# Kernel optimization log

Hardware: AMD Instinct MI355X
Metric: run time of the kernel (lower is better)

The kernel has to match this reference:

```python
import jax, jax.numpy as jnp
import numpy as np

ALPHA = 0.2  # LeakyReLU negative slope
NEG_INF = -9e15


def setup_inputs() -> dict:
    key = jax.random.key(0)
    k1, k2, k3, k4, k5 = jax.random.split(key, 5)
    B, N, F_in, F_out = 1, 8192, 256, 128
    h = jax.random.normal(k1, (B, N, F_in), dtype=jnp.float32)
    adj_mat = jax.random.randint(k2, (B, N, N), 0, 2, dtype=jnp.int32)
    W = jax.random.normal(k3, (F_out, F_in), dtype=jnp.float32) * 0.05
    b = jax.random.normal(k4, (F_out,), dtype=jnp.float32) * 0.05
    a = jax.random.normal(k5, (2 * F_out, 1), dtype=jnp.float32) * 0.05
    return {"h": h, "adj_mat": adj_mat, "W": W, "b": b, "a": a}


def reference(h, adj_mat, W, b, a):
    # Wh: (B, N, F_out)
    Wh = jnp.einsum('bnf,of->bno', h, W) + b
    F_out = W.shape[0]
    # Original builds concat[Wh_i, Wh_j] @ a. Equivalent: a1.Wh_i + a2.Wh_j.
    a1 = a[:F_out, 0]
    a2 = a[F_out:, 0]
    s1 = Wh @ a1  # (B, N) source-i contribution
    s2 = Wh @ a2  # (B, N) source-j contribution
    e = s1[:, :, None] + s2[:, None, :]  # (B, N, N)
    e = jnp.where(e >= 0, e, ALPHA * e)  # LeakyReLU
    e = jnp.where(adj_mat > 0, e, NEG_INF)
    attention = jax.nn.softmax(e, axis=1)  # softmax over dim=1, as in the source
    h_prime = jnp.einsum('bij,bjf->bif', attention, Wh)
    return jax.nn.elu(h_prime)
```

## Files before the change

kernel.cpp:

```cpp
#include <hip/hip_runtime.h>

#define NN 8192
#define FI 256
#define FO 128
#define GAT_ALPHA 0.2f

typedef _Float16 f16x8 __attribute__((ext_vector_type(8)));
typedef _Float16 f16x2 __attribute__((ext_vector_type(2)));
typedef float f32x4 __attribute__((ext_vector_type(4)));
typedef unsigned char uchar;
typedef unsigned int uint32;

__global__ __launch_bounds__(256) void k1_wh(const float* __restrict__ h,
                                             const float* __restrict__ W,
                                             const float* __restrict__ bias,
                                             const float* __restrict__ a,
                                             float* __restrict__ Wh,
                                             float4* __restrict__ r4,
                                             float4* __restrict__ c4,
                                             float2* __restrict__ r2,
                                             _Float16* __restrict__ ey16,
                                             _Float16* __restrict__ ez16,
                                             float* __restrict__ s2x,
                                             float* __restrict__ corr) {
  __shared__ __align__(16) float4 hs4[16][65];
  __shared__ float wt[32][132];
  const int t = threadIdx.x;
  const int j0 = blockIdx.x * 16;
  if (blockIdx.x == 0 && t < FO) corr[t] = 0.f;
#pragma unroll
  for (int e = 0; e < 4; ++e) {
    const int i = t + 256 * e;
    const int row = i >> 6, q = i & 63;
    hs4[row][q] = *(const float4*)(h + (size_t)(j0 + row) * FI + 4 * q);
  }
  const int f4 = (t & 31) * 4;
  const int r0 = (t >> 5) * 2;
  float acc[2][4];
#pragma unroll
  for (int r = 0; r < 2; ++r)
#pragma unroll
    for (int e = 0; e < 4; ++e) acc[r][e] = 0.f;

  for (int kc = 0; kc < FI; kc += 32) {
    __syncthreads();
    {
      const int f = t >> 1, kb = (t & 1) * 16;
      const float* wsrc = W + (size_t)f * FI + kc + kb;
#pragma unroll
      for (int e = 0; e < 4; ++e) {
        const float4 wv = *(const float4*)(wsrc + 4 * e);
        wt[kb + 4 * e + 0][f] = wv.x;
        wt[kb + 4 * e + 1][f] = wv.y;
        wt[kb + 4 * e + 2][f] = wv.z;
        wt[kb + 4 * e + 3][f] = wv.w;
      }
    }
    __syncthreads();
#pragma unroll
    for (int kk = 0; kk < 8; ++kk) {
      float4 wv[4];
#pragma unroll
      for (int i = 0; i < 4; ++i) wv[i] = *(const float4*)&wt[4 * kk + i][f4];
      float4 hv[2];
#pragma unroll
      for (int r = 0; r < 2; ++r) hv[r] = hs4[r0 + r][(kc >> 2) + kk];
#pragma unroll
      for (int r = 0; r < 2; ++r) {
        acc[r][0] += hv[r].x * wv[0].x + hv[r].y * wv[1].x + hv[r].z * wv[2].x + hv[r].w * wv[3].x;
        acc[r][1] += hv[r].x * wv[0].y + hv[r].y * wv[1].y + hv[r].z * wv[2].y + hv[r].w * wv[3].y;
        acc[r][2] += hv[r].x * wv[0].z + hv[r].y * wv[1].z + hv[r].z * wv[2].z + hv[r].w * wv[3].z;
        acc[r][3] += hv[r].x * wv[0].w + hv[r].y * wv[1].w + hv[r].z * wv[2].w + hv[r].w * wv[3].w;
      }
    }
  }
  const float4 bv = *(const float4*)&bias[f4];
  const float4 a1v = *(const float4*)&a[f4];
  const float4 a2v = *(const float4*)&a[FO + f4];
  float s1p[2], s2p[2];
#pragma unroll
  for (int r = 0; r < 2; ++r) {
    float4 o;
    o.x = acc[r][0] + bv.x;
    o.y = acc[r][1] + bv.y;
    o.z = acc[r][2] + bv.z;
    o.w = acc[r][3] + bv.w;
    *(float4*)&Wh[(size_t)(j0 + r0 + r) * FO + f4] = o;
    s1p[r] = o.x * a1v.x + o.y * a1v.y + o.z * a1v.z + o.w * a1v.w;
    s2p[r] = o.x * a2v.x + o.y * a2v.y + o.z * a2v.z + o.w * a2v.w;
  }
#pragma unroll
  for (int m = 16; m >= 1; m >>= 1) {
#pragma unroll
    for (int r = 0; r < 2; ++r) {
      s1p[r] += __shfl_xor(s1p[r], m);
      s2p[r] += __shfl_xor(s2p[r], m);
    }
  }
  if ((t & 31) == 0) {
#pragma unroll
    for (int r = 0; r < 2; ++r) {
      const int j = j0 + r0 + r;
      const float s1 = s1p[r], s2 = s2p[r];
      const float e1 = expf(s1), e1a = expf(GAT_ALPHA * s1);
      const float e2 = expf(s2), e2a = expf(GAT_ALPHA * s2);
      float4 rv; rv.x = s1; rv.y = e1; rv.z = e1a; rv.w = 0.f;
      float4 cv; cv.x = s2; cv.y = e2; cv.z = e2a; cv.w = 0.f;
      r4[j] = rv;
      c4[j] = cv;
      r2[j] = make_float2(e1, e1a);
      ey16[j] = (_Float16)e2;
      ez16[j] = (_Float16)e2a;
      s2x[j] = s2;
    }
  }
}

__global__ __launch_bounds__(256) void k2_stats(const int* __restrict__ adj,
                                                const float4* __restrict__ r4,
                                                const float* __restrict__ s2x,
                                                uchar* __restrict__ bitsB,
                                                float2* __restrict__ zpart) {
  __shared__ float4 rs[64];
  const int t = threadIdx.x;
  const int jc = blockIdx.x & 3;
  const int ic = blockIdx.x >> 2;
  const int i0 = ic * 64;
  const int j0 = jc * 2048 + t * 8;
  if (t < 64) rs[t] = r4[i0 + t];
  const float4 ca = *(const float4*)(s2x + j0);
  const float4 cb = *(const float4*)(s2x + j0 + 4);
  const float cx[8] = {ca.x, ca.y, ca.z, ca.w, cb.x, cb.y, cb.z, cb.w};
  float accP[8], accN[8];
#pragma unroll
  for (int e = 0; e < 8; ++e) { accP[e] = 0.f; accN[e] = 0.f; }
  __syncthreads();
  const int4* ap = (const int4*)(adj + (size_t)i0 * NN + j0);
  uchar* bp = bitsB + (size_t)i0 * (NN / 8) + jc * 256 + t;
  for (int ir = 0; ir < 64; ir += 8) {
    int4 av[8][2];
#pragma unroll
    for (int u = 0; u < 8; ++u) {
      av[u][0] = ap[(size_t)(ir + u) * (NN / 4)];
      av[u][1] = ap[(size_t)(ir + u) * (NN / 4) + 1];
    }
#pragma unroll
    for (int u = 0; u < 8; ++u) {
      const float4 ri = rs[ir + u];
      const int aa[8] = {av[u][0].x, av[u][0].y, av[u][0].z, av[u][0].w,
                         av[u][1].x, av[u][1].y, av[u][1].z, av[u][1].w};
      uint32 byte = 0;
#pragma unroll
      for (int e = 0; e < 8; ++e) {
        const bool act = aa[e] > 0;
        byte |= act ? (1u << e) : 0u;
        const bool pos = (ri.x + cx[e]) >= 0.f;
        accP[e] += (act && pos) ? ri.y : 0.f;
        accN[e] += (act && !pos) ? ri.z : 0.f;
      }
      bp[(size_t)(ir + u) * (NN / 8)] = (uchar)byte;
    }
  }
  float2* zp = zpart + (size_t)ic * NN + j0;
#pragma unroll
  for (int e = 0; e < 8; ++e) zp[e] = make_float2(accP[e], accN[e]);
}

__global__ __launch_bounds__(256) void k3_scale(const float* __restrict__ Wh,
                                                const float4* __restrict__ c4,
                                                const float2* __restrict__ zpart,
                                                _Float16* __restrict__ Wfrag,
                                                float* __restrict__ corr) {
  __shared__ float rz[64];
  __shared__ int emp[64];
  __shared__ float2 psum[256];
  __shared__ __align__(16) _Float16 tile[FO * 64];
  const int t = threadIdx.x;
  const int j0 = blockIdx.x * 64;
  {
    const int jl = t & 63, q = t >> 6;
    float p = 0.f, n = 0.f;
    for (int ic = q * 32; ic < q * 32 + 32; ++ic) {
      const float2 z = zpart[(size_t)ic * NN + j0 + jl];
      p += z.x;
      n += z.y;
    }
    psum[t] = make_float2(p, n);
  }
  __syncthreads();
  if (t < 64) {
    const float p = psum[t].x + psum[64 + t].x + psum[128 + t].x + psum[192 + t].x;
    const float n = psum[t].y + psum[64 + t].y + psum[128 + t].y + psum[192 + t].y;
    const float4 cj = c4[j0 + t];
    const float Z = cj.y * p + cj.z * n;
    rz[t] = (Z > 0.f) ? 1.f / Z : 0.f;
    emp[t] = (Z > 0.f) ? 0 : 1;
  }
  __syncthreads();
  const int f = t & 127, half = t >> 7;
  const unsigned swf = (unsigned)((f & 7) << 4);
  for (int r = half; r < 64; r += 2) {
    const float v = Wh[(size_t)(j0 + r) * FO + f];
    *(_Float16*)((char*)tile + f * 128 + (((unsigned)(r * 2)) ^ swf)) =
        (_Float16)(v * rz[r]);
    if (emp[r]) atomicAdd(&corr[f], v * (1.f / 8192.f));
  }
  __syncthreads();
#pragma unroll
  for (int q = 0; q < 4; ++q) {
    const int G = t + 256 * q;
    const int kcfb = G >> 6, gl = G & 63;
    const int kc = kcfb >> 3, fb = kcfb & 7;
    const int gf = fb * 16 + (gl & 15);
    const int jloc = kc * 32 + (gl >> 4) * 8;
    const f16x8 v = *(const f16x8*)((const char*)tile + gf * 128 +
                                    (((unsigned)(jloc * 2)) ^ ((unsigned)((gf & 7) << 4))));
    ((f16x8*)Wfrag)[(size_t)(((j0 >> 5) + kc) * 8 + fb) * 64 + gl] = v;
  }
}

#define BARRIER_LDS()                                          \
  do {                                                         \
    __builtin_amdgcn_sched_barrier(0);                         \
    asm volatile("s_waitcnt lgkmcnt(0)" ::: "memory");         \
    __builtin_amdgcn_s_barrier();                              \
    __builtin_amdgcn_sched_barrier(0);                         \
  } while (0)

__global__ __launch_bounds__(256) void k4_main(const uchar* __restrict__ bitsB,
                                               const float2* __restrict__ r2,
                                               const _Float16* __restrict__ ey16,
                                               const _Float16* __restrict__ ez16,
                                               const _Float16* __restrict__ Wfrag,
                                               float* __restrict__ part) {
  __shared__ __align__(16) _Float16 P[2][32 * 64];
  __shared__ uint32 lut[256][4];
  const int t = threadIdx.x;
  const int rowtile = blockIdx.x >> 2;
  const int kq = blockIdx.x & 3;
  const int rowbase = rowtile * 32;
  const int koff = kq * 2048;

  {
#pragma unroll
    for (int p = 0; p < 4; ++p) {
      const uint32 lo = ((t >> (2 * p)) & 1) ? 0x0000FFFFu : 0u;
      const uint32 hi = ((t >> (2 * p + 1)) & 1) ? 0xFFFF0000u : 0u;
      lut[t][p] = lo | hi;
    }
  }

  const int pr = t >> 3, jq = t & 7;
  const float2 rr = r2[rowbase + pr];
  const f16x2 rx2 = {(_Float16)rr.x, (_Float16)rr.x};
  const f16x2 ry2 = {(_Float16)rr.y, (_Float16)rr.y};
  const uchar* bp = bitsB + (size_t)(rowbase + pr) * (NN / 8) + (koff >> 3) + jq;
  const _Float16* eyp = ey16 + koff + jq * 8;
  const _Float16* ezp = ez16 + koff + jq * 8;
  char* const pdst0 = (char*)&P[0][0] + pr * 128 + (((unsigned)(jq * 16)) ^ ((unsigned)((pr & 7) << 4)));
  char* const pdst1 = (char*)&P[1][0] + pr * 128 + (((unsigned)(jq * 16)) ^ ((unsigned)((pr & 7) << 4)));

  const int lane = t & 63, wc = t >> 6;
  const int kgrp = lane >> 4, l15 = lane & 15;
  const unsigned asw = (unsigned)((l15 & 7) << 4);
  const int ar0 = l15 * 128;
  const int ar1 = ar0 + 16 * 128;

  f32x4 acc00 = {0.f, 0.f, 0.f, 0.f}, acc01 = {0.f, 0.f, 0.f, 0.f};
  f32x4 acc10 = {0.f, 0.f, 0.f, 0.f}, acc11 = {0.f, 0.f, 0.f, 0.f};

  uchar mb0, mb1;
  uint4 ey0, ez0, ey1, ez1;
  f16x8 B000, B001, B010, B011, B100, B101, B110, B111;

#define LOADALL(S, MB, EY, EZ, Bq00, Bq01, Bq10, Bq11)                              \
  do {                                                                              \
    MB = bp[(S) * 8];                                                               \
    EY = *(const uint4*)(eyp + (S) * 64);                                           \
    EZ = *(const uint4*)(ezp + (S) * 64);                                           \
    const _Float16* _b = Wfrag + ((size_t)((kq * 64 + (S) * 2) * 8 + wc * 2) * 64 + lane) * 8; \
    Bq00 = *(const f16x8*)(_b);                                                     \
    Bq01 = *(const f16x8*)(_b + 512);                                               \
    Bq10 = *(const f16x8*)(_b + 4096);                                              \
    Bq11 = *(const f16x8*)(_b + 4096 + 512);                                        \
  } while (0)

#define PGEN(DST, MB, EY, EZ)                                                        \
  do {                                                                               \
    const uint4 _m = *(const uint4*)(&lut[MB][0]);                                   \
    const uint32 _eys[4] = {EY.x, EY.y, EY.z, EY.w};                                 \
    const uint32 _ezs[4] = {EZ.x, EZ.y, EZ.z, EZ.w};                                 \
    const uint32 _ms[4] = {_m.x, _m.y, _m.z, _m.w};                                  \
    uint32 _o[4];                                                                    \
    _Pragma("unroll") for (int _p = 0; _p < 4; ++_p) {                               \
      const f16x2 _a = __builtin_bit_cast(f16x2, _eys[_p]) * rx2;                    \
      const f16x2 _b2 = __builtin_bit_cast(f16x2, _ezs[_p]) * ry2;                   \
      const f16x2 _mx = __builtin_elementwise_max(_a, _b2);                          \
      _o[_p] = __builtin_bit_cast(uint32, _mx) & _ms[_p];                            \
    }                                                                                \
    uint4 _st; _st.x = _o[0]; _st.y = _o[1]; _st.z = _o[2]; _st.w = _o[3];           \
    *(uint4*)(DST) = _st;                                                            \
  } while (0)

#define DO_MFMA(BUF, Bq00, Bq01, Bq10, Bq11)                                        \
  do {                                                                              \
    const char* _Pb = (const char*)&P[BUF][0];                                      \
    const f16x8 a00 = *(const f16x8*)(_Pb + ar0 + ((((unsigned)(kgrp * 16))) ^ asw));        \
    const f16x8 a01 = *(const f16x8*)(_Pb + ar0 + (((unsigned)(64 + kgrp * 16)) ^ asw));     \
    const f16x8 a10 = *(const f16x8*)(_Pb + ar1 + ((((unsigned)(kgrp * 16))) ^ asw));        \
    const f16x8 a11 = *(const f16x8*)(_Pb + ar1 + (((unsigned)(64 + kgrp * 16)) ^ asw));     \
    __builtin_amdgcn_s_setprio(1);                                                  \
    acc00 = __builtin_amdgcn_mfma_f32_16x16x32_f16(a00, Bq00, acc00, 0, 0, 0);      \
    acc01 = __builtin_amdgcn_mfma_f32_16x16x32_f16(a00, Bq01, acc01, 0, 0, 0);      \
    acc10 = __builtin_amdgcn_mfma_f32_16x16x32_f16(a10, Bq00, acc10, 0, 0, 0);      \
    acc11 = __builtin_amdgcn_mfma_f32_16x16x32_f16(a10, Bq01, acc11, 0, 0, 0);      \
    acc00 = __builtin_amdgcn_mfma_f32_16x16x32_f16(a01, Bq10, acc00, 0, 0, 0);      \
    acc01 = __builtin_amdgcn_mfma_f32_16x16x32_f16(a01, Bq11, acc01, 0, 0, 0);      \
    acc10 = __builtin_amdgcn_mfma_f32_16x16x32_f16(a11, Bq10, acc10, 0, 0, 0);      \
    acc11 = __builtin_amdgcn_mfma_f32_16x16x32_f16(a11, Bq11, acc11, 0, 0, 0);      \
    __builtin_amdgcn_s_setprio(0);                                                  \
  } while (0)

  LOADALL(0, mb0, ey0, ez0, B000, B001, B010, B011);
  LOADALL(1, mb1, ey1, ez1, B100, B101, B110, B111);
  __syncthreads();
  PGEN(pdst0, mb0, ey0, ez0);
  BARRIER_LDS();

  for (int s = 0; s < 32; s += 2) {
    PGEN(pdst1, mb1, ey1, ez1);
    DO_MFMA(0, B000, B001, B010, B011);
    if (s + 2 < 32) LOADALL(s + 2, mb0, ey0, ez0, B000, B001, B010, B011);
    BARRIER_LDS();
    DO_MFMA(1, B100, B101, B110, B111);
    if (s + 2 < 32) PGEN(pdst0, mb0, ey0, ez0);
    if (s + 3 < 32) LOADALL(s + 3, mb1, ey1, ez1, B100, B101, B110, B111);
    BARRIER_LDS();
  }

#undef LOADALL
#undef PGEN
#undef DO_MFMA

  const int orow = rowbase + kgrp * 4;
  const int ocol = wc * 32 + l15;
  float* aP = part + (size_t)kq * NN * FO + (size_t)orow * FO + ocol;
#pragma unroll
  for (int r = 0; r < 4; ++r) {
    aP[(size_t)r * FO] = acc00[r];
    aP[(size_t)r * FO + 16] = acc01[r];
    aP[(size_t)(16 + r) * FO] = acc10[r];
    aP[(size_t)(16 + r) * FO + 16] = acc11[r];
  }
}

__global__ __launch_bounds__(256) void k5_fin(const float* __restrict__ part,
                                              const float* __restrict__ corr,
                                              float* __restrict__ out) {
  const int idx = blockIdx.x * 256 + threadIdx.x;
  const float4 p0 = ((const float4*)part)[idx];
  const float4 p1 = ((const float4*)(part + (size_t)NN * FO))[idx];
  const float4 p2 = ((const float4*)(part + (size_t)2 * NN * FO))[idx];
  const float4 p3 = ((const float4*)(part + (size_t)3 * NN * FO))[idx];
  const float4 c = ((const float4*)corr)[idx & 31];
  float4 v;
  v.x = p0.x + p1.x + p2.x + p3.x + c.x;
  v.y = p0.y + p1.y + p2.y + p3.y + c.y;
  v.z = p0.z + p1.z + p2.z + p3.z + c.z;
  v.w = p0.w + p1.w + p2.w + p3.w + c.w;
  v.x = (v.x > 0.f) ? v.x : (expf(v.x) - 1.f);
  v.y = (v.y > 0.f) ? v.y : (expf(v.y) - 1.f);
  v.z = (v.z > 0.f) ? v.z : (expf(v.z) - 1.f);
  v.w = (v.w > 0.f) ? v.w : (expf(v.w) - 1.f);
  ((float4*)out)[idx] = v;
}

extern "C" void kernel_launch(void* const* d_in, const int* in_sizes, int n_in,
                              void* d_out, int out_size, void* d_ws, size_t ws_size,
                              hipStream_t stream) {
  const float* h = (const float*)d_in[0];
  const int* adj = (const int*)d_in[1];
  const float* W = (const float*)d_in[2];
  const float* b = (const float*)d_in[3];
  const float* a = (const float*)d_in[4];
  float* out = (float*)d_out;
  char* ws = (char*)d_ws;

  float* Wh = (float*)(ws + 0);
  _Float16* Wfrag = (_Float16*)(ws + 0x400000);
  uchar* bits = (uchar*)(ws + 0x600000);
  float2* zpart = (float2*)(ws + 0xE00000);
  float4* r4 = (float4*)(ws + 0x1600000);
  float4* c4 = (float4*)(ws + 0x1620000);
  float2* r2 = (float2*)(ws + 0x1640000);
  _Float16* ey16 = (_Float16*)(ws + 0x1650000);
  _Float16* ez16 = (_Float16*)(ws + 0x1654000);
  float* s2x = (float*)(ws + 0x1658000);
  float* corr = (float*)(ws + 0x1660000);
  float* part = (float*)(ws + 0x1700000);

  k1_wh<<<NN / 16, 256, 0, stream>>>(h, W, b, a, Wh, r4, c4, r2, ey16, ez16, s2x, corr);
  k2_stats<<<512, 256, 0, stream>>>(adj, r4, s2x, bits, zpart);
  k3_scale<<<NN / 64, 256, 0, stream>>>(Wh, c4, zpart, Wfrag, corr);
  k4_main<<<1024, 256, 0, stream>>>(bits, r2, ey16, ez16, Wfrag, part);
  k5_fin<<<(NN * FO / 4) / 256, 256, 0, stream>>>(part, corr, out);
}
```

Before: 119.4 us.

## Compute scores via folded W·a, overlap Wh GEMM with adjacency stats

Scores s1 and s2 are now computed directly from h using precomputed W^T·a1 and W^T·a2 vectors plus a bias constant. This removes the dependency of the adjacency statistics pass on the full Wh GEMM. The Wh GEMM then runs as extra blocks inside a merged kernel alongside the adjacency-scan blocks, so compute-bound and memory-bound work can overlap. In exchange, h is read twice and every score block recomputes the W·a fold, and the folded summation order changes float rounding slightly.

```diff
diff --git a/kernel.cpp b/kernel.cpp
--- a/kernel.cpp
+++ b/kernel.cpp
@@ -11,97 +11,62 @@
 typedef unsigned char uchar;
 typedef unsigned int uint32;
 
-__global__ __launch_bounds__(256) void k1_wh(const float* __restrict__ h,
-                                             const float* __restrict__ W,
-                                             const float* __restrict__ bias,
-                                             const float* __restrict__ a,
-                                             float* __restrict__ Wh,
-                                             float4* __restrict__ r4,
-                                             float4* __restrict__ c4,
-                                             float2* __restrict__ r2,
-                                             _Float16* __restrict__ ey16,
-                                             _Float16* __restrict__ ez16,
-                                             float* __restrict__ s2x,
-                                             float* __restrict__ corr) {
-  __shared__ __align__(16) float4 hs4[16][65];
-  __shared__ float wt[32][132];
+__global__ __launch_bounds__(256) void k1s_scores(const float* __restrict__ h,
+                                                  const float* __restrict__ W,
+                                                  const float* __restrict__ bias,
+                                                  const float* __restrict__ a,
+                                                  float4* __restrict__ r4,
+                                                  float4* __restrict__ c4,
+                                                  float2* __restrict__ r2,
+                                                  _Float16* __restrict__ ey16,
+                                                  _Float16* __restrict__ ez16,
+                                                  float* __restrict__ s2x,
+                                                  float* __restrict__ corr) {
+  __shared__ __align__(16) float wa1[FI];
+  __shared__ __align__(16) float wa2[FI];
+  __shared__ float cb[2];
   const int t = threadIdx.x;
-  const int j0 = blockIdx.x * 16;
+  const int j0 = blockIdx.x * 32;
   if (blockIdx.x == 0 && t < FO) corr[t] = 0.f;
-#pragma unroll
-  for (int e = 0; e < 4; ++e) {
-    const int i = t + 256 * e;
-    const int row = i >> 6, q = i & 63;
-    hs4[row][q] = *(const float4*)(h + (size_t)(j0 + row) * FI + 4 * q);
-  }
-  const int f4 = (t & 31) * 4;
-  const int r0 = (t >> 5) * 2;
-  float acc[2][4];
-#pragma unroll
-  for (int r = 0; r < 2; ++r)
-#pragma unroll
-    for (int e = 0; e < 4; ++e) acc[r][e] = 0.f;
-
-  for (int kc = 0; kc < FI; kc += 32) {
-    __syncthreads();
-    {
-      const int f = t >> 1, kb = (t & 1) * 16;
-      const float* wsrc = W + (size_t)f * FI + kc + kb;
-#pragma unroll
-      for (int e = 0; e < 4; ++e) {
-        const float4 wv = *(const float4*)(wsrc + 4 * e);
-        wt[kb + 4 * e + 0][f] = wv.x;
-        wt[kb + 4 * e + 1][f] = wv.y;
-        wt[kb + 4 * e + 2][f] = wv.z;
-        wt[kb + 4 * e + 3][f] = wv.w;
-      }
-    }
-    __syncthreads();
-#pragma unroll
-    for (int kk = 0; kk < 8; ++kk) {
-      float4 wv[4];
-#pragma unroll
-      for (int i = 0; i < 4; ++i) wv[i] = *(const float4*)&wt[4 * kk + i][f4];
-      float4 hv[2];
-#pragma unroll
-      for (int r = 0; r < 2; ++r) hv[r] = hs4[r0 + r][(kc >> 2) + kk];
-#pragma unroll
-      for (int r = 0; r < 2; ++r) {
-        acc[r][0] += hv[r].x * wv[0].x + hv[r].y * wv[1].x + hv[r].z * wv[2].x + hv[r].w * wv[3].x;
-        acc[r][1] += hv[r].x * wv[0].y + hv[r].y * wv[1].y + hv[r].z * wv[2].y + hv[r].w * wv[3].y;
-        acc[r][2] += hv[r].x * wv[0].z + hv[r].y * wv[1].z + hv[r].z * wv[2].z + hv[r].w * wv[3].z;
-        acc[r][3] += hv[r].x * wv[0].w + hv[r].y * wv[1].w + hv[r].z * wv[2].w + hv[r].w * wv[3].w;
-      }
-    }
-  }
-  const float4 bv = *(const float4*)&bias[f4];
-  const float4 a1v = *(const float4*)&a[f4];
-  const float4 a2v = *(const float4*)&a[FO + f4];
-  float s1p[2], s2p[2];
-#pragma unroll
-  for (int r = 0; r < 2; ++r) {
-    float4 o;
-    o.x = acc[r][0] + bv.x;
-    o.y = acc[r][1] + bv.y;
-    o.z = acc[r][2] + bv.z;
-    o.w = acc[r][3] + bv.w;
-    *(float4*)&Wh[(size_t)(j0 + r0 + r) * FO + f4] = o;
-    s1p[r] = o.x * a1v.x + o.y * a1v.y + o.z * a1v.z + o.w * a1v.w;
-    s2p[r] = o.x * a2v.x + o.y * a2v.y + o.z * a2v.z + o.w * a2v.w;
-  }
-#pragma unroll
-  for (int m = 16; m >= 1; m >>= 1) {
-#pragma unroll
-    for (int r = 0; r < 2; ++r) {
-      s1p[r] += __shfl_xor(s1p[r], m);
-      s2p[r] += __shfl_xor(s2p[r], m);
-    }
-  }
-  if ((t & 31) == 0) {
-#pragma unroll
-    for (int r = 0; r < 2; ++r) {
-      const int j = j0 + r0 + r;
-      const float s1 = s1p[r], s2 = s2p[r];
+  {
+    float sa = 0.f, sb = 0.f;
+    for (int f = 0; f < FO; ++f) {
+      const float w = W[(size_t)f * FI + t];
+      sa += a[f] * w;
+      sb += a[FO + f] * w;
+    }
+    wa1[t] = sa;
+    wa2[t] = sb;
+  }
+  if (t < 64) {
+    float c1 = bias[t] * a[t] + bias[t + 64] * a[t + 64];
+    float c2 = bias[t] * a[FO + t] + bias[t + 64] * a[FO + t + 64];
+#pragma unroll
+    for (int o = 32; o >= 1; o >>= 1) {
+      c1 += __shfl_xor(c1, o);
+      c2 += __shfl_xor(c2, o);
+    }
+    if (t == 0) { cb[0] = c1; cb[1] = c2; }
+  }
+  __syncthreads();
+  const int lane = t & 63, wv = t >> 6;
+  const float4 w1v = *(const float4*)&wa1[lane * 4];
+  const float4 w2v = *(const float4*)&wa2[lane * 4];
+  const float cb1 = cb[0], cb2 = cb[1];
+#pragma unroll
+  for (int rr = 0; rr < 8; ++rr) {
+    const int j = j0 + wv * 8 + rr;
+    const float4 hv = *(const float4*)&h[(size_t)j * FI + lane * 4];
+    float s1 = hv.x * w1v.x + hv.y * w1v.y + hv.z * w1v.z + hv.w * w1v.w;
+    float s2 = hv.x * w2v.x + hv.y * w2v.y + hv.z * w2v.z + hv.w * w2v.w;
+#pragma unroll
+    for (int o = 32; o >= 1; o >>= 1) {
+      s1 += __shfl_xor(s1, o);
+      s2 += __shfl_xor(s2, o);
+    }
+    if (lane == 0) {
+      s1 += cb1;
+      s2 += cb2;
       const float e1 = expf(s1), e1a = expf(GAT_ALPHA * s1);
       const float e2 = expf(s2), e2a = expf(GAT_ALPHA * s2);
       float4 rv; rv.x = s1; rv.y = e1; rv.z = e1a; rv.w = 0.f;
@@ -116,54 +81,124 @@
   }
 }
 
-__global__ __launch_bounds__(256) void k2_stats(const int* __restrict__ adj,
-                                                const float4* __restrict__ r4,
-                                                const float* __restrict__ s2x,
-                                                uchar* __restrict__ bitsB,
-                                                float2* __restrict__ zpart) {
-  __shared__ float4 rs[64];
+__global__ __launch_bounds__(256) void mega(const int* __restrict__ adj,
+                                            const float* __restrict__ h,
+                                            const float* __restrict__ W,
+                                            const float* __restrict__ bias,
+                                            const float4* __restrict__ r4,
+                                            const float* __restrict__ s2x,
+                                            uchar* __restrict__ bitsB,
+                                            float2* __restrict__ zpart,
+                                            float* __restrict__ Wh) {
+  __shared__ __align__(16) char smem[33536];
   const int t = threadIdx.x;
-  const int jc = blockIdx.x & 3;
-  const int ic = blockIdx.x >> 2;
-  const int i0 = ic * 64;
-  const int j0 = jc * 2048 + t * 8;
-  if (t < 64) rs[t] = r4[i0 + t];
-  const float4 ca = *(const float4*)(s2x + j0);
-  const float4 cb = *(const float4*)(s2x + j0 + 4);
-  const float cx[8] = {ca.x, ca.y, ca.z, ca.w, cb.x, cb.y, cb.z, cb.w};
-  float accP[8], accN[8];
-#pragma unroll
-  for (int e = 0; e < 8; ++e) { accP[e] = 0.f; accN[e] = 0.f; }
-  __syncthreads();
-  const int4* ap = (const int4*)(adj + (size_t)i0 * NN + j0);
-  uchar* bp = bitsB + (size_t)i0 * (NN / 8) + jc * 256 + t;
-  for (int ir = 0; ir < 64; ir += 8) {
-    int4 av[8][2];
-#pragma unroll
-    for (int u = 0; u < 8; ++u) {
-      av[u][0] = ap[(size_t)(ir + u) * (NN / 4)];
-      av[u][1] = ap[(size_t)(ir + u) * (NN / 4) + 1];
-    }
-#pragma unroll
-    for (int u = 0; u < 8; ++u) {
-      const float4 ri = rs[ir + u];
-      const int aa[8] = {av[u][0].x, av[u][0].y, av[u][0].z, av[u][0].w,
-                         av[u][1].x, av[u][1].y, av[u][1].z, av[u][1].w};
-      uint32 byte = 0;
-#pragma unroll
-      for (int e = 0; e < 8; ++e) {
-        const bool act = aa[e] > 0;
-        byte |= act ? (1u << e) : 0u;
-        const bool pos = (ri.x + cx[e]) >= 0.f;
-        accP[e] += (act && pos) ? ri.y : 0.f;
-        accN[e] += (act && !pos) ? ri.z : 0.f;
+  if (blockIdx.x < 512) {
+    float4* rs = (float4*)smem;
+    const int jc = blockIdx.x & 3;
+    const int ic = blockIdx.x >> 2;
+    const int i0 = ic * 64;
+    const int j0 = jc * 2048 + t * 8;
+    if (t < 64) rs[t] = r4[i0 + t];
+    const float4 ca = *(const float4*)(s2x + j0);
+    const float4 cbv = *(const float4*)(s2x + j0 + 4);
+    const float cx[8] = {ca.x, ca.y, ca.z, ca.w, cbv.x, cbv.y, cbv.z, cbv.w};
+    float accP[8], accN[8];
+#pragma unroll
+    for (int e = 0; e < 8; ++e) { accP[e] = 0.f; accN[e] = 0.f; }
+    __syncthreads();
+    const int4* ap = (const int4*)(adj + (size_t)i0 * NN + j0);
+    uchar* bp = bitsB + (size_t)i0 * (NN / 8) + jc * 256 + t;
+    for (int ir = 0; ir < 64; ir += 8) {
+      int4 av[8][2];
+#pragma unroll
+      for (int u = 0; u < 8; ++u) {
+        av[u][0] = ap[(size_t)(ir + u) * (NN / 4)];
+        av[u][1] = ap[(size_t)(ir + u) * (NN / 4) + 1];
       }
-      bp[(size_t)(ir + u) * (NN / 8)] = (uchar)byte;
-    }
-  }
-  float2* zp = zpart + (size_t)ic * NN + j0;
-#pragma unroll
-  for (int e = 0; e < 8; ++e) zp[e] = make_float2(accP[e], accN[e]);
+#pragma unroll
+      for (int u = 0; u < 8; ++u) {
+        const float4 ri = rs[ir + u];
+        const int aa[8] = {av[u][0].x, av[u][0].y, av[u][0].z, av[u][0].w,
+                           av[u][1].x, av[u][1].y, av[u][1].z, av[u][1].w};
+        uint32 byte = 0;
+#pragma unroll
+        for (int e = 0; e < 8; ++e) {
+          const bool act = aa[e] > 0;
+          byte |= act ? (1u << e) : 0u;
+          const bool pos = (ri.x + cx[e]) >= 0.f;
+          accP[e] += (act && pos) ? ri.y : 0.f;
+          accN[e] += (act && !pos) ? ri.z : 0.f;
+        }
+        bp[(size_t)(ir + u) * (NN / 8)] = (uchar)byte;
+      }
+    }
+    float2* zp = zpart + (size_t)ic * NN + j0;
+#pragma unroll
+    for (int e = 0; e < 8; ++e) zp[e] = make_float2(accP[e], accN[e]);
+  } else {
+    typedef float4 hs4row_t[65];
+    typedef float wtrow_t[132];
+    hs4row_t* hs4 = (hs4row_t*)smem;
+    wtrow_t* wt = (wtrow_t*)(smem + 16640);
+    const int bid = blockIdx.x - 512;
+    const int j0 = bid * 16;
+#pragma unroll
+    for (int e = 0; e < 4; ++e) {
+      const int i = t + 256 * e;
+      const int row = i >> 6, q = i & 63;
+      hs4[row][q] = *(const float4*)(h + (size_t)(j0 + row) * FI + 4 * q);
+    }
+    const int f4 = (t & 31) * 4;
+    const int r0 = (t >> 5) * 2;
+    float acc[2][4];
+#pragma unroll
+    for (int r = 0; r < 2; ++r)
+#pragma unroll
+      for (int e = 0; e < 4; ++e) acc[r][e] = 0.f;
+
+    for (int kc = 0; kc < FI; kc += 32) {
+      __syncthreads();
+      {
+        const int f = t >> 1, kb = (t & 1) * 16;
+        const float* wsrc = W + (size_t)f * FI + kc + kb;
+#pragma unroll
+        for (int e = 0; e < 4; ++e) {
+          const float4 wv = *(const float4*)(wsrc + 4 * e);
+          wt[kb + 4 * e + 0][f] = wv.x;
+          wt[kb + 4 * e + 1][f] = wv.y;
+          wt[kb + 4 * e + 2][f] = wv.z;
+          wt[kb + 4 * e + 3][f] = wv.w;
+        }
+      }
+      __syncthreads();
+#pragma unroll
+      for (int kk = 0; kk < 8; ++kk) {
+        float4 wv[4];
+#pragma unroll
+        for (int i = 0; i < 4; ++i) wv[i] = *(const float4*)&wt[4 * kk + i][f4];
+        float4 hv[2];
+#pragma unroll
+        for (int r = 0; r < 2; ++r) hv[r] = hs4[r0 + r][(kc >> 2) + kk];
+#pragma unroll
+        for (int r = 0; r < 2; ++r) {
+          acc[r][0] += hv[r].x * wv[0].x + hv[r].y * wv[1].x + hv[r].z * wv[2].x + hv[r].w * wv[3].x;
+          acc[r][1] += hv[r].x * wv[0].y + hv[r].y * wv[1].y + hv[r].z * wv[2].y + hv[r].w * wv[3].y;
+          acc[r][2] += hv[r].x * wv[0].z + hv[r].y * wv[1].z + hv[r].z * wv[2].z + hv[r].w * wv[3].z;
+          acc[r][3] += hv[r].x * wv[0].w + hv[r].y * wv[1].w + hv[r].z * wv[2].w + hv[r].w * wv[3].w;
+        }
+      }
+    }
+    const float4 bv = *(const float4*)&bias[f4];
+#pragma unroll
+    for (int r = 0; r < 2; ++r) {
+      float4 o;
+      o.x = acc[r][0] + bv.x;
+      o.y = acc[r][1] + bv.y;
+      o.z = acc[r][2] + bv.z;
+      o.w = acc[r][3] + bv.w;
+      *(float4*)&Wh[(size_t)(j0 + r0 + r) * FO + f4] = o;
+    }
+  }
 }
 
 __global__ __launch_bounds__(256) void k3_scale(const float* __restrict__ Wh,
@@ -399,8 +434,8 @@
   float* corr = (float*)(ws + 0x1660000);
   float* part = (float*)(ws + 0x1700000);
 
-  k1_wh<<<NN / 16, 256, 0, stream>>>(h, W, b, a, Wh, r4, c4, r2, ey16, ez16, s2x, corr);
-  k2_stats<<<512, 256, 0, stream>>>(adj, r4, s2x, bits, zpart);
+  k1s_scores<<<NN / 32, 256, 0, stream>>>(h, W, b, a, r4, c4, r2, ey16, ez16, s2x, corr);
+  mega<<<1024, 256, 0, stream>>>(adj, h, W, b, r4, s2x, bits, zpart, Wh);
   k3_scale<<<NN / 64, 256, 0, stream>>>(Wh, c4, zpart, Wfrag, corr);
   k4_main<<<1024, 256, 0, stream>>>(bits, r2, ey16, ez16, Wfrag, part);
   k5_fin<<<(NN * FO / 4) / 256, 256, 0, stream>>>(part, corr, out);
```

Measured after the change: 117.5 us (median of 2 runs). No clear change (-1.6%).
